# Performance work log

Measured on AMD Instinct MI355X. Metric: run time of the kernel, lower is better.

Reference implementation:

```python
import jax, jax.numpy as jnp
import numpy as np

H = 12
D_MODEL = 768
H_D = D_MODEL // H


def setup_inputs() -> dict:
    key = jax.random.key(0)
    ks = jax.random.split(key, 11)
    B, S = 2, 2048
    scale_in = 1.0
    w_scale = 1.0 / np.sqrt(D_MODEL)
    inp = {
        "query": jax.random.normal(ks[0], (B, S, D_MODEL), dtype=jnp.float32),
        "key": jax.random.normal(ks[1], (B, S, D_MODEL), dtype=jnp.float32),
        "value": jax.random.normal(ks[2], (B, S, D_MODEL), dtype=jnp.float32),
        "wq": jax.random.normal(ks[3], (D_MODEL, D_MODEL), dtype=jnp.float32) * w_scale,
        "bq": jnp.zeros((D_MODEL,), dtype=jnp.float32),
        "wk": jax.random.normal(ks[4], (D_MODEL, D_MODEL), dtype=jnp.float32) * w_scale,
        "bk": jnp.zeros((D_MODEL,), dtype=jnp.float32),
        "wv": jax.random.normal(ks[5], (D_MODEL, D_MODEL), dtype=jnp.float32) * w_scale,
        "bv": jnp.zeros((D_MODEL,), dtype=jnp.float32),
        "wo": jax.random.normal(ks[6], (D_MODEL, D_MODEL), dtype=jnp.float32) * w_scale,
        "bo": jnp.zeros((D_MODEL,), dtype=jnp.float32),
    }
    return inp


def reference(query, key, value, wq, bq, wk, bk, wv, bv, wo, bo):
    B, S, _ = query.shape
    # QKV projections, split into heads: [B, H, S, h_d]
    def proj(x, w, b):
        y = jnp.einsum("bsd,de->bse", x, w) + b
        return y.reshape(B, S, H, H_D).transpose(0, 2, 1, 3)

    q = proj(query, wq, bq)
    k = proj(key, wk, bk)
    v = proj(value, wv, bv)

    # scaled dot-product attention (dropout disabled / eval mode)
    scores = jnp.einsum("bhsd,bhtd->bhst", q, k) / jnp.sqrt(jnp.float32(H_D))
    wm = jax.nn.softmax(scores, axis=-1)  # [B, H, S, S]
    out = jnp.einsum("bhst,bhtd->bhsd", wm, v)

    # merge heads and output projection
    out = out.transpose(0, 2, 1, 3).reshape(B, S, D_MODEL)
    out = jnp.einsum("bsd,de->bse", out, wo) + bo
    return out
```

## Files before the change

kernel.cpp:

```cpp
#include <hip/hip_runtime.h>

#define H 12
#define DM 768
#define HD 64
#define SEQ 2048
#define BATCH 2
#define MROWS (BATCH*SEQ)

typedef __attribute__((ext_vector_type(8))) short short8;
typedef __attribute__((ext_vector_type(4))) float f32x4;
typedef __attribute__((ext_vector_type(16))) float f32x16;
using u16 = unsigned short;
using u32 = unsigned int;

__device__ __forceinline__ float bf2f(u16 u) { return __uint_as_float(((u32)u) << 16); }
__device__ __forceinline__ u16 f2bf(float x) {
  u32 u = __float_as_uint(x);
  return (u16)((u + 0x7fffu + ((u >> 16) & 1u)) >> 16);
}
__device__ __forceinline__ u32 cvt_pk_bf16(float lo, float hi) {
  u32 r;
  asm("v_cvt_pk_bf16_f32 %0, %1, %2" : "=v"(r) : "v"(lo), "v"(hi));
  return r;
}
__device__ __forceinline__ void gl2lds16(const u16* __restrict__ g, u16* l) {
  __builtin_amdgcn_global_load_lds(
      (const __attribute__((address_space(1))) unsigned int*)g,
      (__attribute__((address_space(3))) unsigned int*)l,
      16, 0, 0);
}

#define C_SM 0.18033688011112042f

__global__ __launch_bounds__(256) void transpose_w4(const float* __restrict__ w0, const float* __restrict__ w1,
                                                    const float* __restrict__ w2, const float* __restrict__ w3,
                                                    u16* __restrict__ dst0)
{
  __shared__ u16 Ts[64][72];
  const float* src = blockIdx.z == 0 ? w0 : blockIdx.z == 1 ? w1 : blockIdx.z == 2 ? w2 : w3;
  u16* dst = dst0 + (size_t)blockIdx.z * DM * DM;
  const int t = threadIdx.x;
  const int r0 = blockIdx.y * 64, c0 = blockIdx.x * 64;
  const int row = t >> 2, cq = (t & 3) * 16;
  const float* sp = src + (size_t)(r0 + row) * DM + c0 + cq;
  #pragma unroll
  for (int g = 0; g < 4; ++g) {
    float4 a = *reinterpret_cast<const float4*>(sp + g * 4);
    Ts[row][cq + g * 4 + 0] = f2bf(a.x);
    Ts[row][cq + g * 4 + 1] = f2bf(a.y);
    Ts[row][cq + g * 4 + 2] = f2bf(a.z);
    Ts[row][cq + g * 4 + 3] = f2bf(a.w);
  }
  __syncthreads();
  union { uint4 v[2]; u16 e[16]; } pk;
  #pragma unroll
  for (int j = 0; j < 16; ++j) pk.e[j] = Ts[cq + j][row];
  uint4* dp = reinterpret_cast<uint4*>(dst + (size_t)(c0 + row) * DM + r0 + cq);
  dp[0] = pk.v[0];
  dp[1] = pk.v[1];
}

template<int BM, bool AF32>
__device__ __forceinline__ void gemm_core(const void* __restrict__ Av, const u16* __restrict__ Bt,
                                          const float* __restrict__ bias, void* __restrict__ dstv,
                                          int mode, int bx, int by, float outScale)
{
  constexpr int AFR = BM / 32;
  constexpr int ACH = BM / 32;
  __shared__ u16 As[BM * 64];
  __shared__ u16 Bs[128 * 64];
  const int t = threadIdx.x;
  const int lane = t & 63, w = t >> 6;
  const int l15 = lane & 15, l4 = lane >> 4;
  const int m0 = by * BM, n0 = bx * 128;
  const int wr = (w >> 1) * (BM / 2), wc = (w & 1) * 64;

  f32x4 acc[AFR][4] = {};

  for (int kt = 0; kt < DM / 64; ++kt) {
    const int k0 = kt * 64;
    #pragma unroll
    for (int c = 0; c < ACH; ++c) {
      const int id = c * 256 + t;
      const int row = id >> 3, xc = id & 7;
      const int db = row * 128 + ((xc * 16) ^ ((row & 7) << 4));
      if (AF32) {
        const float* Af = reinterpret_cast<const float*>(Av) + (size_t)(m0 + row) * DM + k0 + xc * 8;
        float4 a0 = *reinterpret_cast<const float4*>(Af);
        float4 a1 = *reinterpret_cast<const float4*>(Af + 4);
        uint4 v;
        v.x = cvt_pk_bf16(a0.x, a0.y);
        v.y = cvt_pk_bf16(a0.z, a0.w);
        v.z = cvt_pk_bf16(a1.x, a1.y);
        v.w = cvt_pk_bf16(a1.z, a1.w);
        *reinterpret_cast<uint4*>(reinterpret_cast<char*>(As) + db) = v;
      } else {
        uint4 va = *reinterpret_cast<const uint4*>(reinterpret_cast<const u16*>(Av) +
                   (size_t)(m0 + row) * DM + k0 + xc * 8);
        *reinterpret_cast<uint4*>(reinterpret_cast<char*>(As) + db) = va;
      }
    }
    #pragma unroll
    for (int c = 0; c < 4; ++c) {
      const int id = c * 256 + t;
      const int row = id >> 3, xc = id & 7;
      const int db = row * 128 + ((xc * 16) ^ ((row & 7) << 4));
      uint4 vb = *reinterpret_cast<const uint4*>(Bt + (size_t)(n0 + row) * DM + k0 + xc * 8);
      *reinterpret_cast<uint4*>(reinterpret_cast<char*>(Bs) + db) = vb;
    }
    __syncthreads();
    #pragma unroll
    for (int ks = 0; ks < 2; ++ks) {
      short8 ag[AFR], bg[4];
      #pragma unroll
      for (int i = 0; i < AFR; ++i) {
        const int ar = wr + i * 16 + l15;
        ag[i] = *reinterpret_cast<const short8*>(reinterpret_cast<const char*>(As) +
                 ar * 128 + ((ks * 64 + l4 * 16) ^ ((ar & 7) << 4)));
      }
      #pragma unroll
      for (int j = 0; j < 4; ++j) {
        const int br = wc + j * 16 + l15;
        bg[j] = *reinterpret_cast<const short8*>(reinterpret_cast<const char*>(Bs) +
                 br * 128 + ((ks * 64 + l4 * 16) ^ ((br & 7) << 4)));
      }
      #pragma unroll
      for (int i = 0; i < AFR; ++i)
        #pragma unroll
        for (int j = 0; j < 4; ++j)
          acc[i][j] = __builtin_amdgcn_mfma_f32_16x16x32_bf16(ag[i], bg[j], acc[i][j], 0, 0, 0);
    }
    __syncthreads();
  }

  #pragma unroll
  for (int j = 0; j < 4; ++j) {
    const int gcol = n0 + wc + j * 16 + l15;
    const float bb = bias[gcol];
    #pragma unroll
    for (int i = 0; i < AFR; ++i) {
      const int grow = m0 + wr + i * 16 + l4 * 4;
      if (mode == 2) {
        float* dst = reinterpret_cast<float*>(dstv);
        #pragma unroll
        for (int r = 0; r < 4; ++r)
          dst[(size_t)(grow + r) * DM + gcol] = acc[i][j][r] + bb;
      } else {
        u16* dst = reinterpret_cast<u16*>(dstv);
        const int b = grow >> 11, s = grow & (SEQ - 1);
        const int h = gcol >> 6, d = gcol & 63;
        if (mode == 0) {
          #pragma unroll
          for (int r = 0; r < 4; ++r)
            dst[((size_t)(b * H + h) * SEQ + s + r) * HD + d] = f2bf((acc[i][j][r] + bb) * outScale);
        } else {
          union { uint2 v; u16 e[4]; } pk;
          #pragma unroll
          for (int r = 0; r < 4; ++r) pk.e[r] = f2bf(acc[i][j][r] + bb);
          *reinterpret_cast<uint2*>(dst + ((size_t)(b * H + h) * HD + d) * SEQ + s) = pk.v;
        }
      }
    }
  }
}

__global__ __launch_bounds__(256) void gemm_qkv_kernel(
    const float* __restrict__ xq, const float* __restrict__ xk, const float* __restrict__ xv,
    const u16* __restrict__ wT, const float* __restrict__ bq, const float* __restrict__ bk,
    const float* __restrict__ bv, u16* __restrict__ Qb, u16* __restrict__ Kb, u16* __restrict__ Vtb)
{
  const int flat = blockIdx.z * 384 + blockIdx.y * 6 + blockIdx.x;
  const int nb = (flat & 7) * 144 + (flat >> 3);
  const int z = nb / 384, rem = nb % 384;
  const int by = rem / 6, bx = rem % 6;
  const float* A    = z == 0 ? xq : z == 1 ? xk : xv;
  const u16* Bt     = wT + (size_t)z * DM * DM;
  const float* bias = z == 0 ? bq : z == 1 ? bk : bv;
  u16* dst          = z == 0 ? Qb : z == 1 ? Kb : Vtb;
  const float sc    = z == 1 ? C_SM : 1.0f;
  gemm_core<64, true>(A, Bt, bias, dst, z == 2 ? 1 : 0, bx, by, sc);
}

__global__ __launch_bounds__(256) void gemm_o_kernel(const u16* __restrict__ A, const u16* __restrict__ woT,
                                                     const float* __restrict__ bo, float* __restrict__ out)
{
  const int flat = blockIdx.y * 6 + blockIdx.x;
  const int nb = (flat & 7) * 96 + (flat >> 3);
  gemm_core<32, false>(A, woT, bo, out, 2, nb % 6, nb / 6, 1.0f);
}

__global__ __launch_bounds__(256) void attn_kernel(const u16* __restrict__ Q, const u16* __restrict__ K,
                                                   const u16* __restrict__ Vt,
                                                   float* __restrict__ Op0, float* __restrict__ Op1,
                                                   float* __restrict__ Lp0, float* __restrict__ Lp1)
{
  __shared__ u16 Ks[3][64 * 64];
  __shared__ u16 Vs[3][64 * 64];
  const int t = threadIdx.x;
  const int lane = t & 63, w = t >> 6;
  const int l31 = lane & 31, hi = lane >> 5;
  const int flat = blockIdx.y * 32 + blockIdx.x;
  const int nbid = (flat & 7) * 96 + (flat >> 3);
  const int bh = nbid >> 5;
  const int rem = nbid & 31;
  const int q0 = (rem >> 1) * 128;
  const int half = rem & 1;
  const int kv0 = half * (SEQ / 2);
  const size_t qbase  = ((size_t)bh * SEQ + q0) * HD;
  const size_t kbase0 = (size_t)bh * SEQ * HD;
  const size_t vtbase = (size_t)bh * HD * SEQ;
  float* __restrict__ Op = half ? Op1 : Op0;
  float* __restrict__ Lp = half ? Lp1 : Lp0;
  constexpr int NT = SEQ / 2 / 64;

  const int r8 = lane >> 3;
  const int pcol = ((lane & 7) ^ r8) * 8;

  short8 qf[4];
  {
    const u16* qp = Q + qbase + (size_t)(w * 32 + l31) * HD + hi * 8;
    #pragma unroll
    for (int ks = 0; ks < 4; ++ks)
      qf[ks] = *reinterpret_cast<const short8*>(qp + ks * 16);
  }

  auto STAGE = [&](int pt, int buf) {
    #pragma unroll
    for (int j = 0; j < 2; ++j) {
      const int ci = w * 2 + j;
      const int row = ci * 8 + r8;
      gl2lds16(K + kbase0 + (size_t)(kv0 + pt * 64 + row) * HD + pcol, &Ks[buf][ci * 512]);
      gl2lds16(Vt + vtbase + (size_t)row * SEQ + kv0 + pt * 64 + pcol, &Vs[buf][ci * 512]);
    }
  };

  STAGE(0, 0);
  STAGE(1, 1);

  short8 ones;
  #pragma unroll
  for (int j = 0; j < 8; ++j) ones[j] = (short)0x3F80;

  f32x16 oacc[2] = {};
  f32x16 accL = {};
  int cur = 0;

  for (int kt = 0; kt < NT; ++kt) {
    asm volatile("s_waitcnt vmcnt(4)" ::: "memory");
    __builtin_amdgcn_s_barrier();

    {
      const int pt = (kt + 2) & (NT - 1);
      const int pbuf = (cur + 2) % 3;
      STAGE(pt, pbuf);
    }

    f32x16 s0 = {}, s1 = {};
    __builtin_amdgcn_s_setprio(1);
    #pragma unroll
    for (int ks = 0; ks < 4; ++ks) {
      const int cb = ks * 32 + hi * 16;
      short8 kf0 = *reinterpret_cast<const short8*>(reinterpret_cast<const char*>(Ks[cur]) +
                   l31 * 128 + (cb ^ ((l31 & 7) << 4)));
      short8 kf1 = *reinterpret_cast<const short8*>(reinterpret_cast<const char*>(Ks[cur]) +
                   (32 + l31) * 128 + (cb ^ ((l31 & 7) << 4)));
      s0 = __builtin_amdgcn_mfma_f32_32x32x16_bf16(kf0, qf[ks], s0, 0, 0, 0);
      s1 = __builtin_amdgcn_mfma_f32_32x32x16_bf16(kf1, qf[ks], s1, 0, 0, 0);
    }
    __builtin_amdgcn_s_setprio(0);

    float p0[16], p1[16];
    #pragma unroll
    for (int r = 0; r < 16; ++r) {
      p0[r] = exp2f(s0[r]);
      p1[r] = exp2f(s1[r]);
    }

    __builtin_amdgcn_s_setprio(1);
    #pragma unroll
    for (int ks2 = 0; ks2 < 4; ++ks2) {
      const float* P = (ks2 < 2) ? p0 : p1;
      const int ro = (ks2 & 1) * 8;
      u32 a0 = cvt_pk_bf16(P[ro + 0], P[ro + 1]);
      u32 a1 = cvt_pk_bf16(P[ro + 2], P[ro + 3]);
      u32 b0 = cvt_pk_bf16(P[ro + 4], P[ro + 5]);
      u32 b1 = cvt_pk_bf16(P[ro + 6], P[ro + 7]);
      asm volatile("v_permlane32_swap_b32 %0, %1" : "+v"(a0), "+v"(b0));
      asm volatile("v_permlane32_swap_b32 %0, %1" : "+v"(a1), "+v"(b1));
      union { u32 u[4]; short8 s; } pa;
      pa.u[0] = a0; pa.u[1] = a1; pa.u[2] = b0; pa.u[3] = b1;
      accL = __builtin_amdgcn_mfma_f32_32x32x16_bf16(pa.s, ones, accL, 0, 0, 0);
      #pragma unroll
      for (int dt = 0; dt < 2; ++dt) {
        const int vr = dt * 32 + l31;
        short8 vf = *reinterpret_cast<const short8*>(reinterpret_cast<const char*>(Vs[cur]) +
                    vr * 128 + ((ks2 * 32 + hi * 16) ^ ((vr & 7) << 4)));
        oacc[dt] = __builtin_amdgcn_mfma_f32_32x32x16_bf16(pa.s, vf, oacc[dt], 0, 0, 0);
      }
    }
    __builtin_amdgcn_s_setprio(0);
    cur = (cur == 2) ? 0 : cur + 1;
  }

  if (l31 == 0) {
    #pragma unroll
    for (int r = 0; r < 16; ++r) {
      const int qo = (r & 3) + 8 * (r >> 2) + 4 * hi;
      Lp[(size_t)bh * SEQ + q0 + w * 32 + qo] = accL[r];
    }
  }
  #pragma unroll
  for (int r = 0; r < 16; ++r) {
    const int qo = (r & 3) + 8 * (r >> 2) + 4 * hi;
    const size_t base = ((size_t)bh * SEQ + q0 + w * 32 + qo) * HD;
    Op[base + l31]      = oacc[0][r];
    Op[base + 32 + l31] = oacc[1][r];
  }
}

__global__ __launch_bounds__(256) void attn_merge(const float* __restrict__ Op0, const float* __restrict__ Op1,
                                                  const float* __restrict__ Lp0, const float* __restrict__ Lp1,
                                                  u16* __restrict__ Ab)
{
  const int id = blockIdx.x * 256 + threadIdx.x;
  const int row = id >> 4, dc = (id & 15) * 4;
  const int bh = row >> 11, q = row & (SEQ - 1);
  const int b = bh / H, h = bh % H;
  const float inv = 1.f / (Lp0[row] + Lp1[row]);
  float4 o0 = *reinterpret_cast<const float4*>(Op0 + (size_t)row * HD + dc);
  float4 o1 = *reinterpret_cast<const float4*>(Op1 + (size_t)row * HD + dc);
  uint2 o;
  o.x = cvt_pk_bf16((o0.x + o1.x) * inv, (o0.y + o1.y) * inv);
  o.y = cvt_pk_bf16((o0.z + o1.z) * inv, (o0.w + o1.w) * inv);
  *reinterpret_cast<uint2*>(Ab + ((size_t)(b * SEQ + q)) * DM + h * HD + dc) = o;
}

extern "C" void kernel_launch(void* const* d_in, const int* in_sizes, int n_in,
                              void* d_out, int out_size, void* d_ws, size_t ws_size,
                              hipStream_t stream)
{
  const float* q  = (const float*)d_in[0];
  const float* k  = (const float*)d_in[1];
  const float* v  = (const float*)d_in[2];
  const float* wq = (const float*)d_in[3];
  const float* bq = (const float*)d_in[4];
  const float* wk = (const float*)d_in[5];
  const float* bk = (const float*)d_in[6];
  const float* wv = (const float*)d_in[7];
  const float* bv = (const float*)d_in[8];
  const float* wo = (const float*)d_in[9];
  const float* bo = (const float*)d_in[10];

  u16* ws = (u16*)d_ws;
  const size_t WSZ = (size_t)DM * DM;
  const size_t TSZ = (size_t)MROWS * DM;
  const size_t NQ  = (size_t)BATCH * H * SEQ;
  u16* wT  = ws;
  u16* Qb  = ws + 4 * WSZ;
  u16* Kb  = Qb + TSZ;
  u16* Vtb = Kb + TSZ;
  u16* Ab  = Vtb + TSZ;
  float* Op0 = (float*)(Ab + TSZ);
  float* Op1 = Op0 + TSZ;
  float* Lp0 = Op1 + TSZ;
  float* Lp1 = Lp0 + NQ;

  transpose_w4<<<dim3(12, 12, 4), 256, 0, stream>>>(wq, wk, wv, wo, wT);
  gemm_qkv_kernel<<<dim3(6, 64, 3), 256, 0, stream>>>(q, k, v, wT, bq, bk, bv, Qb, Kb, Vtb);
  attn_kernel<<<dim3(32, 24), 256, 0, stream>>>(Qb, Kb, Vtb, Op0, Op1, Lp0, Lp1);
  attn_merge<<<dim3((int)(NQ * 16 / 256)), 256, 0, stream>>>(Op0, Op1, Lp0, Lp1, Ab);
  gemm_o_kernel<<<dim3(6, 128), 256, 0, stream>>>(Ab, wT + 3 * WSZ, bo, (float*)d_out);
}
```

Before: 108.2 us.

## Fuse split-KV merge into attention kernel via atomic last-block reduction

```diff
diff --git a/kernel.cpp b/kernel.cpp
--- a/kernel.cpp
+++ b/kernel.cpp
@@ -21,6 +21,11 @@
 __device__ __forceinline__ u32 cvt_pk_bf16(float lo, float hi) {
   u32 r;
   asm("v_cvt_pk_bf16_f32 %0, %1, %2" : "=v"(r) : "v"(lo), "v"(hi));
+  return r;
+}
+__device__ __forceinline__ float fexp2(float x) {
+  float r;
+  asm("v_exp_f32 %0, %1" : "=v"(r) : "v"(x));
   return r;
 }
 __device__ __forceinline__ void gl2lds16(const u16* __restrict__ g, u16* l) {
@@ -192,7 +197,8 @@
 __global__ __launch_bounds__(256) void attn_kernel(const u16* __restrict__ Q, const u16* __restrict__ K,
                                                    const u16* __restrict__ Vt,
                                                    float* __restrict__ Op0, float* __restrict__ Op1,
-                                                   float* __restrict__ Lp0, float* __restrict__ Lp1)
+                                                   float* __restrict__ Lp0, float* __restrict__ Lp1,
+                                                   u32* __restrict__ cnt, u16* __restrict__ Ab)
 {
   __shared__ u16 Ks[3][64 * 64];
   __shared__ u16 Vs[3][64 * 64];
@@ -272,8 +278,8 @@
     float p0[16], p1[16];
     #pragma unroll
     for (int r = 0; r < 16; ++r) {
-      p0[r] = exp2f(s0[r]);
-      p1[r] = exp2f(s1[r]);
+      p0[r] = fexp2(s0[r]);
+      p1[r] = fexp2(s1[r]);
     }
 
     __builtin_amdgcn_s_setprio(1);
@@ -316,23 +322,30 @@
     Op[base + l31]      = oacc[0][r];
     Op[base + 32 + l31] = oacc[1][r];
   }
-}
-
-__global__ __launch_bounds__(256) void attn_merge(const float* __restrict__ Op0, const float* __restrict__ Op1,
-                                                  const float* __restrict__ Lp0, const float* __restrict__ Lp1,
-                                                  u16* __restrict__ Ab)
-{
-  const int id = blockIdx.x * 256 + threadIdx.x;
-  const int row = id >> 4, dc = (id & 15) * 4;
-  const int bh = row >> 11, q = row & (SEQ - 1);
-  const int b = bh / H, h = bh % H;
-  const float inv = 1.f / (Lp0[row] + Lp1[row]);
-  float4 o0 = *reinterpret_cast<const float4*>(Op0 + (size_t)row * HD + dc);
-  float4 o1 = *reinterpret_cast<const float4*>(Op1 + (size_t)row * HD + dc);
-  uint2 o;
-  o.x = cvt_pk_bf16((o0.x + o1.x) * inv, (o0.y + o1.y) * inv);
-  o.y = cvt_pk_bf16((o0.z + o1.z) * inv, (o0.w + o1.w) * inv);
-  *reinterpret_cast<uint2*>(Ab + ((size_t)(b * SEQ + q)) * DM + h * HD + dc) = o;
+
+  __syncthreads();
+  __shared__ u32 who;
+  if (t == 0) {
+    who = __hip_atomic_fetch_add(&cnt[nbid >> 1], 1u, __ATOMIC_ACQ_REL, __HIP_MEMORY_SCOPE_AGENT);
+  }
+  __syncthreads();
+  if (who == 1) {
+    const float* __restrict__ Po = half ? Op0 : Op1;
+    const float* __restrict__ Pl = half ? Lp0 : Lp1;
+    const int b = bh / H, h = bh % H;
+    #pragma unroll
+    for (int r = 0; r < 16; ++r) {
+      const int qo = (r & 3) + 8 * (r >> 2) + 4 * hi;
+      const size_t rowq = (size_t)bh * SEQ + q0 + w * 32 + qo;
+      const float inv = 1.f / (accL[r] + Pl[rowq]);
+      const float o0 = (oacc[0][r] + Po[rowq * HD + l31]) * inv;
+      const float o1 = (oacc[1][r] + Po[rowq * HD + 32 + l31]) * inv;
+      const int qg = q0 + w * 32 + qo;
+      const size_t obase = ((size_t)(b * SEQ + qg)) * DM + h * HD;
+      Ab[obase + l31]      = f2bf(o0);
+      Ab[obase + 32 + l31] = f2bf(o1);
+    }
+  }
 }
 
 extern "C" void kernel_launch(void* const* d_in, const int* in_sizes, int n_in,
@@ -364,10 +377,11 @@
   float* Op1 = Op0 + TSZ;
   float* Lp0 = Op1 + TSZ;
   float* Lp1 = Lp0 + NQ;
-
+  u32* cnt  = (u32*)(Lp1 + NQ);
+
+  hipMemsetAsync(cnt, 0, 384 * sizeof(u32), stream);
   transpose_w4<<<dim3(12, 12, 4), 256, 0, stream>>>(wq, wk, wv, wo, wT);
   gemm_qkv_kernel<<<dim3(6, 64, 3), 256, 0, stream>>>(q, k, v, wT, bq, bk, bv, Qb, Kb, Vtb);
-  attn_kernel<<<dim3(32, 24), 256, 0, stream>>>(Qb, Kb, Vtb, Op0, Op1, Lp0, Lp1);
-  attn_merge<<<dim3((int)(NQ * 16 / 256)), 256, 0, stream>>>(Op0, Op1, Lp0, Lp1, Ab);
+  attn_kernel<<<dim3(32, 24), 256, 0, stream>>>(Qb, Kb, Vtb, Op0, Op1, Lp0, Lp1, cnt, Ab);
   gemm_o_kernel<<<dim3(6, 128), 256, 0, stream>>>(Ab, wT + 3 * WSZ, bo, (float*)d_out);
 }
```

New measurement: 138.1 us. 27.7% more time.
